# Optimization experiments

Hardware: AMD Instinct MI355X
Metric: run time of the kernel (lower is better)

The kernel has to match this reference:

```python
import jax, jax.numpy as jnp
import numpy as np


def setup_inputs() -> dict:
    key = jax.random.key(0)
    ks = jax.random.split(key, 8)
    B, n_users, n_items, F = 4096, 20000, 10000, 64
    return {
        "user_idx": jax.random.randint(ks[0], (B,), 0, n_users),
        "item_idx": jax.random.randint(ks[1], (B,), 0, n_items),
        "interactions": jax.random.randint(ks[2], (n_users + 1, n_items + 1), 0, 2).astype(jnp.int32),
        "user_embed_w": jax.random.normal(ks[3], (n_users + 1, F), jnp.float32) * 0.01,
        "item_embed_w": jax.random.normal(ks[4], (n_items + 1, F), jnp.float32) * 0.01,
        "proj_u_w": jax.random.normal(ks[5], (F, n_items), jnp.float32) * 0.01,
        "proj_i_w": jax.random.normal(ks[6], (F, n_users), jnp.float32) * 0.01,
        "logit_w": jax.random.normal(ks[7], (1, F), jnp.float32) * 0.1,
        "logit_b": jnp.zeros((1,), jnp.float32),
    }


def _hist_proj(slice_int, mask_col, proj_w):
    # slice_int: (B, N) int rows; zero out the target column per-row, sum, project, scale
    B = slice_int.shape[0]
    s = slice_int.astype(jnp.float32)
    s = s.at[jnp.arange(B), mask_col].set(0.0)
    ssum = jnp.clip(jnp.sum(s, axis=1, keepdims=True), 1.0, None)  # (B,1)
    return (s @ proj_w.T) / jnp.sqrt(ssum)  # (B,F)


def reference(user_idx, item_idx, interactions, user_embed_w, item_embed_w,
              proj_u_w, proj_i_w, logit_w, logit_b):
    # history paths: gather rows, mask the (u,i) entry, sum-normalize, dense project
    user_hist = _hist_proj(interactions[user_idx, :-1], item_idx, proj_u_w)      # (B,F)
    item_hist = _hist_proj(interactions.T[item_idx, :-1], user_idx, proj_i_w)    # (B,F)
    rep_user = user_embed_w[user_idx] + user_hist
    rep_item = item_embed_w[item_idx] + item_hist
    pred_vector = rep_user * rep_item                                            # GMF
    logit = pred_vector @ logit_w.T + logit_b                                    # (B,1)
    return logit[:, 0]
```

## Files before the change

kernel.cpp:

```cpp
#include <hip/hip_runtime.h>
#include <hip/hip_bf16.h>
#include <stdint.h>

#define B    4096
#define NU   20000
#define NI   10000
#define RS   10001
#define XAS  320
#define XTS  640
#define NKI  625
#define NKU  313
#define SPI  32
#define SPU  16
#define KCH  20

typedef __attribute__((ext_vector_type(8))) short bf16x8;
typedef __attribute__((ext_vector_type(4))) float f32x4;

__global__ __launch_bounds__(256) void k_packall(const int* __restrict__ X,
                                                 uint32_t* __restrict__ Xall) {
  int lane = threadIdx.x & 63, wv = threadIdx.x >> 6;
  int u = blockIdx.x * 4 + wv;
  const int* row = X + (size_t)u * RS;
  uint32_t* dst = Xall + (size_t)u * XAS;
  if (lane < 7) dst[313 + lane] = 0u;
  for (int it = 0; it < 40; ++it) {
    int c0 = it * 256 + lane * 4;
    int v0, v1, v2, v3;
    if (it < 39) {
      v0 = row[c0]; v1 = row[c0 + 1]; v2 = row[c0 + 2]; v3 = row[c0 + 3];
    } else {
      v0 = (c0     < NI) ? row[c0]     : 0;
      v1 = (c0 + 1 < NI) ? row[c0 + 1] : 0;
      v2 = (c0 + 2 < NI) ? row[c0 + 2] : 0;
      v3 = (c0 + 3 < NI) ? row[c0 + 3] : 0;
    }
    uint32_t nib = (v0 ? 1u : 0u) | (v1 ? 2u : 0u) | (v2 ? 4u : 0u) | (v3 ? 8u : 0u);
    uint32_t acc = nib << ((lane & 7) * 4);
    acc |= __shfl_xor(acc, 1);
    acc |= __shfl_xor(acc, 2);
    acc |= __shfl_xor(acc, 4);
    int k = it * 8 + (lane >> 3);
    if ((lane & 7) == 0 && k < 313) dst[k] = acc;
  }
}

__global__ __launch_bounds__(256) void k_bitT(const uint32_t* __restrict__ Xall,
                                              uint32_t* __restrict__ XallT) {
  __shared__ uint32_t ilo[512][9], ihi[512][9];
  __shared__ uint32_t olo[512][9], ohi[512][9];
  int t = threadIdx.x;
  int lane = t & 63, wd = t >> 6;
  int W0 = blockIdx.x * 8;
  int u0 = blockIdx.y * 512;
  int rr = t >> 3, w = t & 7;
  const unsigned long long* Xq = (const unsigned long long*)Xall;
  unsigned long long* Tq = (unsigned long long*)XallT;
  for (int i = 0; i < 16; ++i) {
    int r = rr + 32 * i;
    int u = u0 + r;
    unsigned long long v = (u < NU) ? Xq[(size_t)u * (XAS / 2) + W0 + w] : 0ULL;
    ilo[r][w] = (uint32_t)v;
    ihi[r][w] = (uint32_t)(v >> 32);
  }
  __syncthreads();
  const unsigned long long ML[6] = {
    0x5555555555555555ULL, 0x3333333333333333ULL, 0x0F0F0F0F0F0F0F0FULL,
    0x00FF00FF00FF00FFULL, 0x0000FFFF0000FFFFULL, 0x00000000FFFFFFFFULL };
  for (int i = 0; i < 16; ++i) {
    int tile = wd * 16 + i;
    int c = tile >> 3, W = tile & 7;
    int rowi = c * 64 + lane;
    unsigned long long x = ((unsigned long long)ihi[rowi][W] << 32) | ilo[rowi][W];
#pragma unroll
    for (int lv = 0; lv < 6; ++lv) {
      int s = 1 << lv;
      unsigned long long m = ML[lv];
      uint32_t xl = (uint32_t)x, xh = (uint32_t)(x >> 32);
      unsigned long long y = ((unsigned long long)__shfl_xor(xh, s) << 32) |
                             (uint32_t)__shfl_xor(xl, s);
      x = (lane & s) ? ((x & ~m) | ((y & ~m) >> s))
                     : ((x & m) | ((y & m) << s));
    }
    int rowo = W * 64 + lane;
    olo[rowo][c] = (uint32_t)x;
    ohi[rowo][c] = (uint32_t)(x >> 32);
  }
  __syncthreads();
  for (int i = 0; i < 16; ++i) {
    int r = rr + 32 * i;
    int j = W0 * 64 + r;
    unsigned long long v = ((unsigned long long)ohi[r][w] << 32) | olo[r][w];
    Tq[(size_t)j * (XTS / 2) + blockIdx.y * 8 + w] = v;
  }
}

__global__ __launch_bounds__(256) void k_prepW2(const float* __restrict__ pi,
    const float* __restrict__ pu, uint4* __restrict__ WfI, uint4* __restrict__ WfU) {
  __shared__ float tile[64][33];
  const float* src; uint4* wfrag; int NSRC, ks;
  if (blockIdx.x < NKI) { src = pi; wfrag = WfI; NSRC = NU; ks = blockIdx.x; }
  else                  { src = pu; wfrag = WfU; NSRC = NI; ks = blockIdx.x - NKI; }
  int tid = threadIdx.x;
  {
    int f = tid >> 2, part = tid & 3;
    int ubase = ks * 32 + part * 8;
    const float* sp = src + (size_t)f * NSRC;
#pragma unroll
    for (int q = 0; q < 8; q++) {
      int u = ubase + q;
      tile[f][part * 8 + q] = (u < NSRC) ? sp[u] : 0.f;
    }
  }
  __syncthreads();
  int l = tid & 63, t = tid >> 6;
  int g = l >> 4, f = t * 16 + (l & 15);
  int u0 = g * 8;
  uint32_t w[4];
#pragma unroll
  for (int p = 0; p < 4; p++) {
    __hip_bfloat16 blo = __float2bfloat16(tile[f][u0 + 2 * p]);
    __hip_bfloat16 bhi = __float2bfloat16(tile[f][u0 + 2 * p + 1]);
    w[p] = (uint32_t)*(uint16_t*)&blo | ((uint32_t)*(uint16_t*)&bhi << 16);
  }
  wfrag[(size_t)ks * 256 + tid] = make_uint4(w[0], w[1], w[2], w[3]);
}

__global__ __launch_bounds__(256) void k_mfma2(
    const uint32_t* __restrict__ XallT, const uint32_t* __restrict__ Xall,
    const uint4* __restrict__ WfI, const uint4* __restrict__ WfU,
    const int* __restrict__ item_idx, const int* __restrict__ user_idx,
    float* __restrict__ partFI, float* __restrict__ partFU) {
  int lane = threadIdx.x & 63, wid = threadIdx.x >> 6;
  const uint32_t* bits; const uint4* wf; float* pf; const int* idx;
  int bstride, nk, seg, pair;
  if (blockIdx.x < 1024) {
    pair = blockIdx.x & 31; seg = blockIdx.x >> 5;
    bits = XallT; bstride = XTS; wf = WfI; pf = partFI; idx = item_idx; nk = NKI;
  } else {
    int bx = blockIdx.x - 1024;
    pair = bx & 31; seg = bx >> 5;
    bits = Xall; bstride = XAS; wf = WfU; pf = partFU; idx = user_idx; nk = NKU;
  }
  int b0 = pair * 128 + wid * 32;
  int r0 = b0 + (lane & 15);
  int g = lane >> 4;
  int kbeg = seg * KCH, kend = min(nk, kbeg + KCH);
  const uint32_t* brow0 = bits + (size_t)idx[r0] * bstride;
  const uint32_t* brow1 = bits + (size_t)idx[r0 + 16] * bstride;
  f32x4 acc0[4] = {{0,0,0,0},{0,0,0,0},{0,0,0,0},{0,0,0,0}};
  f32x4 acc1[4] = {{0,0,0,0},{0,0,0,0},{0,0,0,0},{0,0,0,0}};
  for (int ks = kbeg; ks < kend; ++ks) {
    uint32_t by0 = (brow0[ks] >> (g * 8)) & 0xffu;
    uint32_t by1 = (brow1[ks] >> (g * 8)) & 0xffu;
    union { bf16x8 v; uint32_t u[4]; } A0, A1;
#pragma unroll
    for (int p = 0; p < 4; p++) {
      A0.u[p] = (((by0 >> (2 * p)) & 1u) ? 0x3F80u : 0u) |
                (((by0 >> (2 * p + 1)) & 1u) ? 0x3F800000u : 0u);
      A1.u[p] = (((by1 >> (2 * p)) & 1u) ? 0x3F80u : 0u) |
                (((by1 >> (2 * p + 1)) & 1u) ? 0x3F800000u : 0u);
    }
    const uint4* wp = wf + (size_t)ks * 256 + lane;
#pragma unroll
    for (int t = 0; t < 4; t++) {
      union { bf16x8 v; uint4 q; } Bf;
      Bf.q = wp[t * 64];
      acc0[t] = __builtin_amdgcn_mfma_f32_16x16x32_bf16(A0.v, Bf.v, acc0[t], 0, 0, 0);
      acc1[t] = __builtin_amdgcn_mfma_f32_16x16x32_bf16(A1.v, Bf.v, acc1[t], 0, 0, 0);
    }
  }
#pragma unroll
  for (int t = 0; t < 4; t++)
#pragma unroll
    for (int r = 0; r < 4; r++) {
      int b = b0 + (lane >> 4) * 4 + r;
      int f = t * 16 + (lane & 15);
      pf[((size_t)seg * B + b) * 64 + f] = acc0[t][r];
      pf[((size_t)seg * B + (b + 16)) * 64 + f] = acc1[t][r];
    }
}

__global__ __launch_bounds__(256) void k_final(
    const float* __restrict__ partFI, const float* __restrict__ partFU,
    const uint32_t* __restrict__ XallT, const uint32_t* __restrict__ Xall,
    const int* __restrict__ user_idx, const int* __restrict__ item_idx,
    const int* __restrict__ X, const float* __restrict__ pi, const float* __restrict__ pu,
    const float* __restrict__ uew, const float* __restrict__ iew,
    const float* __restrict__ lw, const float* __restrict__ lb,
    float* __restrict__ out) {
  int gid = blockIdx.x * 256 + threadIdx.x;
  int b = gid >> 6, f = gid & 63;
  int u = user_idx[b], it = item_idx[b];
  float ai = 0.f, au = 0.f;
  for (int s = 0; s < SPI; s++) ai += partFI[((size_t)s * B + b) * 64 + f];
  for (int s = 0; s < SPU; s++) au += partFU[((size_t)s * B + b) * 64 + f];
  const uint32_t* rowi = XallT + (size_t)it * XTS;
  const uint32_t* rowu = Xall + (size_t)u * XAS;
  int ci = 0, cu = 0;
  for (int d = f; d < NKI; d += 64) ci += __popc(rowi[d]);
  for (int d = f; d < NKU; d += 64) cu += __popc(rowu[d]);
  for (int off = 32; off; off >>= 1) {
    ci += __shfl_xor(ci, off);
    cu += __shfl_xor(cu, off);
  }
  int xc = X[(size_t)u * RS + it];
  if (xc) {
    ai -= pi[(size_t)f * NU + u];  ci -= 1;
    au -= pu[(size_t)f * NI + it]; cu -= 1;
  }
  float di = (float)ci; if (di < 1.f) di = 1.f;
  float du = (float)cu; if (du < 1.f) du = 1.f;
  float repi = iew[(size_t)it * 64 + f] + ai / sqrtf(di);
  float repu = uew[(size_t)u * 64 + f] + au / sqrtf(du);
  float v = repu * repi * lw[f];
  for (int off = 32; off; off >>= 1) v += __shfl_xor(v, off);
  if ((threadIdx.x & 63) == 0) out[b] = v + lb[0];
}

extern "C" void kernel_launch(void* const* d_in, const int* in_sizes, int n_in,
                              void* d_out, int out_size, void* d_ws, size_t ws_size,
                              hipStream_t stream) {
  const int*   user_idx = (const int*)d_in[0];
  const int*   item_idx = (const int*)d_in[1];
  const int*   X        = (const int*)d_in[2];
  const float* uew      = (const float*)d_in[3];
  const float* iew      = (const float*)d_in[4];
  const float* pu       = (const float*)d_in[5];
  const float* pi       = (const float*)d_in[6];
  const float* lw       = (const float*)d_in[7];
  const float* lb       = (const float*)d_in[8];
  float* out = (float*)d_out;

  char* wsb = (char*)d_ws;
  uint32_t* Xall   = (uint32_t*)(wsb + 0);
  uint32_t* XallT  = (uint32_t*)(wsb + 25600000);
  uint4*    WfI    = (uint4*)(wsb + 51814400);
  uint4*    WfU    = (uint4*)(wsb + 54374400);
  float*    partFI = (float*)(wsb + 55656448);
  float*    partFU = (float*)(wsb + 89210880);

  k_prepW2<<<NKI + NKU, 256, 0, stream>>>(pi, pu, WfI, WfU);
  k_packall<<<5000, 256, 0, stream>>>(X, Xall);
  k_bitT<<<dim3(20, 40), 256, 0, stream>>>(Xall, XallT);
  k_mfma2<<<1536, 256, 0, stream>>>(XallT, Xall, WfI, WfU, item_idx, user_idx,
                                    partFI, partFU);
  k_final<<<1024, 256, 0, stream>>>(partFI, partFU, XallT, Xall,
                                    user_idx, item_idx, X, pi, pu, uew, iew, lw, lb, out);
}
```

Measured before the change: 304.1 us.

## Pack interaction matrix as flat bitstream with 16-byte loads, then realign per row

```diff
diff --git a/kernel.cpp b/kernel.cpp
--- a/kernel.cpp
+++ b/kernel.cpp
@@ -13,36 +13,44 @@
 #define SPI  32
 #define SPU  16
 #define KCH  20
+#define NCHUNK 781329
 
 typedef __attribute__((ext_vector_type(8))) short bf16x8;
 typedef __attribute__((ext_vector_type(4))) float f32x4;
 
-__global__ __launch_bounds__(256) void k_packall(const int* __restrict__ X,
-                                                 uint32_t* __restrict__ Xall) {
-  int lane = threadIdx.x & 63, wv = threadIdx.x >> 6;
-  int u = blockIdx.x * 4 + wv;
-  const int* row = X + (size_t)u * RS;
-  uint32_t* dst = Xall + (size_t)u * XAS;
-  if (lane < 7) dst[313 + lane] = 0u;
-  for (int it = 0; it < 40; ++it) {
-    int c0 = it * 256 + lane * 4;
-    int v0, v1, v2, v3;
-    if (it < 39) {
-      v0 = row[c0]; v1 = row[c0 + 1]; v2 = row[c0 + 2]; v3 = row[c0 + 3];
-    } else {
-      v0 = (c0     < NI) ? row[c0]     : 0;
-      v1 = (c0 + 1 < NI) ? row[c0 + 1] : 0;
-      v2 = (c0 + 2 < NI) ? row[c0 + 2] : 0;
-      v3 = (c0 + 3 < NI) ? row[c0 + 3] : 0;
-    }
-    uint32_t nib = (v0 ? 1u : 0u) | (v1 ? 2u : 0u) | (v2 ? 4u : 0u) | (v3 ? 8u : 0u);
+__global__ __launch_bounds__(256) void k_packflat(const int* __restrict__ X,
+                                                  uint32_t* __restrict__ Xflat) {
+  int wid = threadIdx.x >> 6, lane = threadIdx.x & 63;
+  int wg = blockIdx.x * 4 + wid;
+  const uint4* Xv = (const uint4*)X;
+#pragma unroll 2
+  for (int c = wg; c < NCHUNK; c += 4096) {
+    uint4 v = Xv[(size_t)c * 64 + lane];
+    uint32_t nib = (v.x ? 1u : 0u) | (v.y ? 2u : 0u) | (v.z ? 4u : 0u) | (v.w ? 8u : 0u);
     uint32_t acc = nib << ((lane & 7) * 4);
     acc |= __shfl_xor(acc, 1);
     acc |= __shfl_xor(acc, 2);
     acc |= __shfl_xor(acc, 4);
-    int k = it * 8 + (lane >> 3);
-    if ((lane & 7) == 0 && k < 313) dst[k] = acc;
-  }
+    if ((lane & 7) == 0) Xflat[(size_t)c * 8 + (lane >> 3)] = acc;
+  }
+}
+
+__global__ __launch_bounds__(256) void k_realign(const uint32_t* __restrict__ Xflat,
+                                                 uint32_t* __restrict__ Xall) {
+  int gid = blockIdx.x * 256 + threadIdx.x;
+  int u = gid / 320;
+  int k = gid - u * 320;
+  uint32_t val = 0;
+  if (k < 313) {
+    size_t a = (size_t)u * RS;
+    size_t W0 = (a >> 5) + k;
+    int s = (int)(a & 31);
+    uint32_t lo = Xflat[W0];
+    uint32_t hi = Xflat[W0 + 1];
+    val = s ? ((lo >> s) | (hi << (32 - s))) : lo;
+    if (k == 312) val &= 0xFFFFu;
+  }
+  Xall[gid] = val;
 }
 
 __global__ __launch_bounds__(256) void k_bitT(const uint32_t* __restrict__ Xall,
@@ -239,9 +247,11 @@
   uint4*    WfU    = (uint4*)(wsb + 54374400);
   float*    partFI = (float*)(wsb + 55656448);
   float*    partFU = (float*)(wsb + 89210880);
+  uint32_t* Xflat  = (uint32_t*)partFI;
 
   k_prepW2<<<NKI + NKU, 256, 0, stream>>>(pi, pu, WfI, WfU);
-  k_packall<<<5000, 256, 0, stream>>>(X, Xall);
+  k_packflat<<<1024, 256, 0, stream>>>(X, Xflat);
+  k_realign<<<25000, 256, 0, stream>>>(Xflat, Xall);
   k_bitT<<<dim3(20, 40), 256, 0, stream>>>(Xall, XallT);
   k_mfma2<<<1536, 256, 0, stream>>>(XallT, Xall, WfI, WfU, item_idx, user_idx,
                                     partFI, partFU);
```

Result: no change. 308.0 us (+1.3%).
